# Kernel tuning notes

Hardware: AMD Instinct MI355X
Metric: run time of the kernel (lower is better)

Reference implementation:

```python
import jax, jax.numpy as jnp
import numpy as np

B, T, S, D = 8, 32, 256, 1024


def setup_inputs() -> dict:
    key = jax.random.key(0)
    ks = jax.random.split(key, 10)
    scale = 1.0 / np.sqrt(D)
    return {
        "source1": jax.random.normal(ks[0], (B, T, D), jnp.float32),
        "source2": jax.random.normal(ks[1], (B, T, D), jnp.float32),
        "memory_bank": jax.random.normal(ks[2], (B, S, D), jnp.float32),
        "source_masks1": jnp.ones((B, T), jnp.float32),
        "source_masks2": jnp.ones((B, T), jnp.float32),
        "W_q1": jax.random.normal(ks[3], (D, D), jnp.float32) * scale,
        "b_q1": jnp.zeros((D,), jnp.float32),
        "W_q2": jax.random.normal(ks[4], (D, D), jnp.float32) * scale,
        "b_q2": jnp.zeros((D,), jnp.float32),
        "W_cate": jax.random.normal(ks[5], (2, 2 * D), jnp.float32) * scale,
        "b_cate": jnp.zeros((2,), jnp.float32),
        "W_v": jax.random.normal(ks[6], (D, D), jnp.float32) * scale,
    }


def reference(source1, source2, memory_bank, source_masks1, source_masks2,
              W_q1, b_q1, W_q2, b_q2, W_cate, b_cate, W_v):
    Bq, Tq, Dd = source1.shape
    # accumulate(): running prefix-mean over the segment axis, then mask.
    denom = jnp.arange(1, Tq + 1, dtype=source1.dtype)[None, :, None]
    s1 = (jnp.cumsum(source1, axis=1) / denom) * source_masks1[:, :, None]
    s2 = (jnp.cumsum(source2, axis=1) / denom) * source_masks2[:, :, None]
    # score(): gated attention scoring.
    q1 = s1 @ W_q1.T + b_q1  # [B,T,D]
    q2 = s2 @ W_q2.T + b_q2  # [B,T,D]
    # tanh gate broadcast over all (tgt, src) pairs -> [B,T,S,D]
    g = jnp.tanh(q1[:, :, None, :] + q2[:, :, None, :] + memory_bank[:, None, :, :])
    # sum_j (g @ W_v.T)[..., j] == g @ sum_j W_v[j, :]
    w_colsum = jnp.sum(W_v, axis=0)              # [D]
    sum_gate = g @ w_colsum                       # [B,T,S]
    # linear_cate(concat([h_s, sum_gate*h_s])) split into two halves
    pa = memory_bank @ W_cate[:, :Dd].T           # [B,S,2]
    pb = memory_bank @ W_cate[:, Dd:].T           # [B,S,2]
    out = pa[:, None, :, :] + sum_gate[..., None] * pb[:, None, :, :] + b_cate
    return out  # [B,T,S,2]
```

## Files before the change

kernel.cpp:

```cpp
#include <hip/hip_runtime.h>
#include <hip/hip_bf16.h>

#define Bb 8
#define Tt 32
#define Ss 256
#define Dd 1024

typedef short short8 __attribute__((ext_vector_type(8)));
typedef float floatx4 __attribute__((ext_vector_type(4)));

__device__ __forceinline__ float tanh_fast(float x) {
    x = fminf(12.f, fmaxf(-12.f, x));
    float e = __expf(2.f * x);
    return 1.f - 2.f * __builtin_amdgcn_rcpf(e + 1.f);
}

__device__ __forceinline__ float dot4(float4 a, float4 b) {
    return a.x * b.x + a.y * b.y + a.z * b.z + a.w * b.w;
}

__global__ __launch_bounds__(256) void prefix_kernel(
        const float* __restrict__ src1, const float* __restrict__ src2,
        const float* __restrict__ m1, const float* __restrict__ m2,
        __hip_bfloat16* __restrict__ s1b, __hip_bfloat16* __restrict__ s2b) {
    int idx = blockIdx.x * 256 + threadIdx.x;
    int srcsel = idx >> 13;
    int bd = idx & 8191;
    int b = bd >> 10, d = bd & 1023;
    const float* sp = srcsel ? src2 : src1;
    const float* mp = srcsel ? m2 : m1;
    __hip_bfloat16* op = srcsel ? s2b : s1b;
    float a = 0.f;
    for (int t = 0; t < Tt; t++) {
        a += sp[(size_t)(b * Tt + t) * Dd + d];
        float inv = __builtin_amdgcn_rcpf((float)(t + 1));
        op[(size_t)(b * Tt + t) * Dd + d] = __float2bfloat16(a * inv * mp[b * Tt + t]);
    }
}

__global__ __launch_bounds__(256) void castw_kernel(
        const float* __restrict__ W1, const float* __restrict__ W2,
        __hip_bfloat16* __restrict__ W1b, __hip_bfloat16* __restrict__ W2b) {
    int i = blockIdx.x * 256 + threadIdx.x;
    W1b[i] = __float2bfloat16(W1[i]);
    W2b[i] = __float2bfloat16(W2[i]);
}

__global__ __launch_bounds__(256) void wsum_part_kernel(
        const float* __restrict__ Wv, float* __restrict__ part) {
    int db = blockIdx.x & 3;
    int jc = blockIdx.x >> 2;
    int d = db * 256 + threadIdx.x;
    float a = 0.f;
    int j0 = jc * 64;
    for (int j = 0; j < 64; j++)
        a += Wv[(size_t)(j0 + j) * Dd + d];
    part[jc * Dd + d] = a;
}

__global__ __launch_bounds__(256) void wsum_final_kernel(
        const float* __restrict__ part, float* __restrict__ wsum) {
    int d = blockIdx.x * 256 + threadIdx.x;
    float a = 0.f;
    #pragma unroll
    for (int jc = 0; jc < 16; jc++)
        a += part[jc * Dd + d];
    wsum[d] = a;
}

__global__ __launch_bounds__(256) void gemm_kernel(
        const __hip_bfloat16* __restrict__ s1b, const __hip_bfloat16* __restrict__ s2b,
        const __hip_bfloat16* __restrict__ W1b, const __hip_bfloat16* __restrict__ W2b,
        const float* __restrict__ bq1, const float* __restrict__ bq2,
        float* __restrict__ q) {
    const int wave = threadIdx.x >> 6;
    const int lane = threadIdx.x & 63;
    const int tile = blockIdx.x * 4 + wave;
    const int m0 = (tile & 15) * 16;
    const int n0 = (tile >> 4) * 16;
    const int lm = lane & 15;
    const int quad = lane >> 4;

    floatx4 acc1 = {0.f, 0.f, 0.f, 0.f};
    floatx4 acc2 = {0.f, 0.f, 0.f, 0.f};
    const __hip_bfloat16* arow1 = s1b + (size_t)(m0 + lm) * Dd;
    const __hip_bfloat16* arow2 = s2b + (size_t)(m0 + lm) * Dd;
    const __hip_bfloat16* brow1 = W1b + (size_t)(n0 + lm) * Dd;
    const __hip_bfloat16* brow2 = W2b + (size_t)(n0 + lm) * Dd;

    for (int k0 = 0; k0 < Dd; k0 += 32) {
        const int off = k0 + quad * 8;
        short8 a1 = *(const short8*)(arow1 + off);
        short8 b1 = *(const short8*)(brow1 + off);
        acc1 = __builtin_amdgcn_mfma_f32_16x16x32_bf16(a1, b1, acc1, 0, 0, 0);
        short8 a2 = *(const short8*)(arow2 + off);
        short8 b2 = *(const short8*)(brow2 + off);
        acc2 = __builtin_amdgcn_mfma_f32_16x16x32_bf16(a2, b2, acc2, 0, 0, 0);
    }

    const int n = n0 + lm;
    const float bias = bq1[n] + bq2[n];
    #pragma unroll
    for (int r = 0; r < 4; r++) {
        const int m = m0 + quad * 4 + r;
        q[(size_t)m * Dd + n] = acc1[r] + acc2[r] + bias;
    }
}

__global__ __launch_bounds__(256) void out_kernel(
        const float* __restrict__ q, const float* __restrict__ mem,
        const float* __restrict__ wsum, const float* __restrict__ Wc,
        const float* __restrict__ bc, float* __restrict__ out) {
    const int wave = threadIdx.x >> 6;
    const int lane = threadIdx.x & 63;
    const int gid = blockIdx.x * 4 + wave;
    const int b = gid >> 8;
    const int s = gid & 255;
    const float* mrow = mem + (size_t)gid * Dd;

    float4 mv[4], wv[4];
    float pa0 = 0.f, pa1 = 0.f, pb0 = 0.f, pb1 = 0.f;
    #pragma unroll
    for (int j = 0; j < 4; j++) {
        const int d0 = j * 256 + lane * 4;
        mv[j] = *(const float4*)(mrow + d0);
        wv[j] = *(const float4*)(wsum + d0);
        float4 wa0 = *(const float4*)(Wc + d0);
        float4 wa1 = *(const float4*)(Wc + 2048 + d0);
        float4 wb0 = *(const float4*)(Wc + 1024 + d0);
        float4 wb1 = *(const float4*)(Wc + 2048 + 1024 + d0);
        pa0 += dot4(mv[j], wa0);
        pa1 += dot4(mv[j], wa1);
        pb0 += dot4(mv[j], wb0);
        pb1 += dot4(mv[j], wb1);
    }
    #pragma unroll
    for (int o = 32; o > 0; o >>= 1) {
        pa0 += __shfl_xor(pa0, o);
        pa1 += __shfl_xor(pa1, o);
        pb0 += __shfl_xor(pb0, o);
        pb1 += __shfl_xor(pb1, o);
    }
    const float bc0 = bc[0], bc1 = bc[1];

    for (int t = 0; t < Tt; t++) {
        const float* qrow = q + (size_t)(b * Tt + t) * Dd;
        float p = 0.f;
        #pragma unroll
        for (int j = 0; j < 4; j++) {
            const int d0 = j * 256 + lane * 4;
            float4 qv = *(const float4*)(qrow + d0);
            p = fmaf(tanh_fast(qv.x + mv[j].x), wv[j].x, p);
            p = fmaf(tanh_fast(qv.y + mv[j].y), wv[j].y, p);
            p = fmaf(tanh_fast(qv.z + mv[j].z), wv[j].z, p);
            p = fmaf(tanh_fast(qv.w + mv[j].w), wv[j].w, p);
        }
        #pragma unroll
        for (int o = 32; o > 0; o >>= 1) p += __shfl_xor(p, o);
        if (lane == 0) {
            const size_t o2 = ((size_t)(b * Tt + t) * Ss + s) * 2;
            out[o2]     = pa0 + p * pb0 + bc0;
            out[o2 + 1] = pa1 + p * pb1 + bc1;
        }
    }
}

extern "C" void kernel_launch(void* const* d_in, const int* in_sizes, int n_in,
                              void* d_out, int out_size, void* d_ws, size_t ws_size,
                              hipStream_t stream) {
    const float* src1 = (const float*)d_in[0];
    const float* src2 = (const float*)d_in[1];
    const float* mem  = (const float*)d_in[2];
    const float* m1   = (const float*)d_in[3];
    const float* m2   = (const float*)d_in[4];
    const float* Wq1  = (const float*)d_in[5];
    const float* bq1  = (const float*)d_in[6];
    const float* Wq2  = (const float*)d_in[7];
    const float* bq2  = (const float*)d_in[8];
    const float* Wc   = (const float*)d_in[9];
    const float* bc   = (const float*)d_in[10];
    const float* Wv   = (const float*)d_in[11];
    float* out = (float*)d_out;

    char* ws = (char*)d_ws;
    __hip_bfloat16* s1b = (__hip_bfloat16*)(ws);
    __hip_bfloat16* s2b = (__hip_bfloat16*)(ws + (512u << 10));
    __hip_bfloat16* W1b = (__hip_bfloat16*)(ws + (1u << 20));
    __hip_bfloat16* W2b = (__hip_bfloat16*)(ws + (3u << 20));
    float* q    = (float*)(ws + (5u << 20));
    float* wsum = (float*)(ws + (6u << 20));
    float* part = (float*)(ws + (6u << 20) + 4096);

    prefix_kernel<<<64, 256, 0, stream>>>(src1, src2, m1, m2, s1b, s2b);
    castw_kernel<<<4096, 256, 0, stream>>>(Wq1, Wq2, W1b, W2b);
    wsum_part_kernel<<<64, 256, 0, stream>>>(Wv, part);
    wsum_final_kernel<<<4, 256, 0, stream>>>(part, wsum);
    gemm_kernel<<<256, 256, 0, stream>>>(s1b, s2b, W1b, W2b, bq1, bq2, q);
    out_kernel<<<512, 256, 0, stream>>>(q, mem, wsum, Wc, bc, out);
}
```

Measured before the change: 147.1 us.

## Merge prep kernels, widen GEMM tiles, and rewrite tanh gate as sigmoid

The prefix-mean, weight cast and partial column-sum launches are folded into one prep kernel, and the final column-sum reduction is folded into the GEMM launch, cutting six launches to three. The GEMM now uses one wave per block, each computing a 16x32 tile and accumulating both weight products into shared accumulators. The tanh is rewritten as 1 - 2*sigmoid with the 2*log2(e) scale pre-applied to q and memory, so each element costs one exp2 and one rcp; the constant part is folded into per-row constants. The out kernel splits the T dimension in half to double the block count and processes two t rows per iteration with vectorised float2 stores. The clamp is removed, so exp2 can overflow to inf for large inputs, which rcp then maps to zero.

```diff
diff --git a/kernel.cpp b/kernel.cpp
--- a/kernel.cpp
+++ b/kernel.cpp
@@ -5,134 +5,155 @@
 #define Tt 32
 #define Ss 256
 #define Dd 1024
+#define SCALE 2.885390081777927f
 
 typedef short short8 __attribute__((ext_vector_type(8)));
 typedef float floatx4 __attribute__((ext_vector_type(4)));
 
-__device__ __forceinline__ float tanh_fast(float x) {
-    x = fminf(12.f, fmaxf(-12.f, x));
-    float e = __expf(2.f * x);
-    return 1.f - 2.f * __builtin_amdgcn_rcpf(e + 1.f);
+__device__ __forceinline__ unsigned short bf16b(float x) {
+    __hip_bfloat16 h = __float2bfloat16(x);
+    return *(unsigned short*)&h;
 }
 
 __device__ __forceinline__ float dot4(float4 a, float4 b) {
     return a.x * b.x + a.y * b.y + a.z * b.z + a.w * b.w;
 }
 
-__global__ __launch_bounds__(256) void prefix_kernel(
+__device__ __forceinline__ float sigm_term(float q, float m, float w, float acc) {
+    float e = __builtin_amdgcn_exp2f(q + m);
+    return fmaf(w, __builtin_amdgcn_rcpf(e + 1.f), acc);
+}
+
+__global__ __launch_bounds__(256) void prep_kernel(
         const float* __restrict__ src1, const float* __restrict__ src2,
         const float* __restrict__ m1, const float* __restrict__ m2,
-        __hip_bfloat16* __restrict__ s1b, __hip_bfloat16* __restrict__ s2b) {
-    int idx = blockIdx.x * 256 + threadIdx.x;
-    int srcsel = idx >> 13;
-    int bd = idx & 8191;
-    int b = bd >> 10, d = bd & 1023;
-    const float* sp = srcsel ? src2 : src1;
-    const float* mp = srcsel ? m2 : m1;
-    __hip_bfloat16* op = srcsel ? s2b : s1b;
-    float a = 0.f;
-    for (int t = 0; t < Tt; t++) {
-        a += sp[(size_t)(b * Tt + t) * Dd + d];
-        float inv = __builtin_amdgcn_rcpf((float)(t + 1));
-        op[(size_t)(b * Tt + t) * Dd + d] = __float2bfloat16(a * inv * mp[b * Tt + t]);
-    }
-}
-
-__global__ __launch_bounds__(256) void castw_kernel(
         const float* __restrict__ W1, const float* __restrict__ W2,
-        __hip_bfloat16* __restrict__ W1b, __hip_bfloat16* __restrict__ W2b) {
-    int i = blockIdx.x * 256 + threadIdx.x;
-    W1b[i] = __float2bfloat16(W1[i]);
-    W2b[i] = __float2bfloat16(W2[i]);
-}
-
-__global__ __launch_bounds__(256) void wsum_part_kernel(
-        const float* __restrict__ Wv, float* __restrict__ part) {
-    int db = blockIdx.x & 3;
-    int jc = blockIdx.x >> 2;
-    int d = db * 256 + threadIdx.x;
-    float a = 0.f;
-    int j0 = jc * 64;
-    for (int j = 0; j < 64; j++)
-        a += Wv[(size_t)(j0 + j) * Dd + d];
-    part[jc * Dd + d] = a;
-}
-
-__global__ __launch_bounds__(256) void wsum_final_kernel(
-        const float* __restrict__ part, float* __restrict__ wsum) {
-    int d = blockIdx.x * 256 + threadIdx.x;
-    float a = 0.f;
-    #pragma unroll
-    for (int jc = 0; jc < 16; jc++)
-        a += part[jc * Dd + d];
-    wsum[d] = a;
-}
-
-__global__ __launch_bounds__(256) void gemm_kernel(
-        const __hip_bfloat16* __restrict__ s1b, const __hip_bfloat16* __restrict__ s2b,
-        const __hip_bfloat16* __restrict__ W1b, const __hip_bfloat16* __restrict__ W2b,
+        const float* __restrict__ Wv,
+        unsigned short* __restrict__ W1b, unsigned short* __restrict__ W2b,
+        unsigned short* __restrict__ s1b, unsigned short* __restrict__ s2b,
+        float* __restrict__ part) {
+    const int blk = blockIdx.x, tid = threadIdx.x;
+    if (blk < 1024) {
+        const int idx = blk * 256 + tid;
+        float4 a = ((const float4*)W1)[idx];
+        float4 b = ((const float4*)W2)[idx];
+        ushort4 oa = { bf16b(a.x), bf16b(a.y), bf16b(a.z), bf16b(a.w) };
+        ushort4 ob = { bf16b(b.x), bf16b(b.y), bf16b(b.z), bf16b(b.w) };
+        ((ushort4*)W1b)[idx] = oa;
+        ((ushort4*)W2b)[idx] = ob;
+    } else if (blk < 1088) {
+        const int bb = blk - 1024;
+        const int db = bb & 3, jc = bb >> 2;
+        const int d = db * 256 + tid;
+        float a = 0.f;
+        const int j0 = jc * 64;
+        for (int j = 0; j < 64; j++)
+            a += Wv[(size_t)(j0 + j) * Dd + d];
+        part[jc * Dd + d] = a;
+    } else {
+        const int idx = (blk - 1088) * 256 + tid;
+        const int srcsel = idx >> 13;
+        const int bd = idx & 8191;
+        const int b = bd >> 10, d = bd & 1023;
+        const float* sp = srcsel ? src2 : src1;
+        const float* mp = srcsel ? m2 : m1;
+        unsigned short* op = srcsel ? s2b : s1b;
+        float a = 0.f;
+        for (int t = 0; t < Tt; t++) {
+            a += sp[(size_t)(b * Tt + t) * Dd + d];
+            float inv = __builtin_amdgcn_rcpf((float)(t + 1));
+            op[(size_t)(b * Tt + t) * Dd + d] = bf16b(a * inv * mp[b * Tt + t]);
+        }
+    }
+}
+
+__global__ __launch_bounds__(64) void gemm_kernel(
+        const unsigned short* __restrict__ s1b, const unsigned short* __restrict__ s2b,
+        const unsigned short* __restrict__ W1b, const unsigned short* __restrict__ W2b,
         const float* __restrict__ bq1, const float* __restrict__ bq2,
-        float* __restrict__ q) {
-    const int wave = threadIdx.x >> 6;
-    const int lane = threadIdx.x & 63;
-    const int tile = blockIdx.x * 4 + wave;
-    const int m0 = (tile & 15) * 16;
-    const int n0 = (tile >> 4) * 16;
+        const float* __restrict__ part,
+        float* __restrict__ qp, float* __restrict__ wsum) {
+    const int blk = blockIdx.x;
+    const int lane = threadIdx.x;
+    if (blk >= 512) {
+        const int d = (blk - 512) * 64 + lane;
+        float a = 0.f;
+        #pragma unroll
+        for (int jc = 0; jc < 16; jc++)
+            a += part[jc * Dd + d];
+        wsum[d] = a;
+        return;
+    }
+    const int m0 = (blk & 15) * 16;
+    const int n0 = (blk >> 4) * 32;
     const int lm = lane & 15;
     const int quad = lane >> 4;
 
+    floatx4 acc0 = {0.f, 0.f, 0.f, 0.f};
     floatx4 acc1 = {0.f, 0.f, 0.f, 0.f};
-    floatx4 acc2 = {0.f, 0.f, 0.f, 0.f};
-    const __hip_bfloat16* arow1 = s1b + (size_t)(m0 + lm) * Dd;
-    const __hip_bfloat16* arow2 = s2b + (size_t)(m0 + lm) * Dd;
-    const __hip_bfloat16* brow1 = W1b + (size_t)(n0 + lm) * Dd;
-    const __hip_bfloat16* brow2 = W2b + (size_t)(n0 + lm) * Dd;
-
+    const unsigned short* a1p = s1b + (size_t)(m0 + lm) * Dd;
+    const unsigned short* a2p = s2b + (size_t)(m0 + lm) * Dd;
+    const unsigned short* b1a = W1b + (size_t)(n0 + lm) * Dd;
+    const unsigned short* b1b = W1b + (size_t)(n0 + 16 + lm) * Dd;
+    const unsigned short* b2a = W2b + (size_t)(n0 + lm) * Dd;
+    const unsigned short* b2b = W2b + (size_t)(n0 + 16 + lm) * Dd;
+
+    #pragma unroll 2
     for (int k0 = 0; k0 < Dd; k0 += 32) {
         const int off = k0 + quad * 8;
-        short8 a1 = *(const short8*)(arow1 + off);
-        short8 b1 = *(const short8*)(brow1 + off);
-        acc1 = __builtin_amdgcn_mfma_f32_16x16x32_bf16(a1, b1, acc1, 0, 0, 0);
-        short8 a2 = *(const short8*)(arow2 + off);
-        short8 b2 = *(const short8*)(brow2 + off);
-        acc2 = __builtin_amdgcn_mfma_f32_16x16x32_bf16(a2, b2, acc2, 0, 0, 0);
-    }
-
-    const int n = n0 + lm;
-    const float bias = bq1[n] + bq2[n];
+        short8 a1 = *(const short8*)(a1p + off);
+        short8 a2 = *(const short8*)(a2p + off);
+        short8 vb1a = *(const short8*)(b1a + off);
+        short8 vb2a = *(const short8*)(b2a + off);
+        short8 vb1b = *(const short8*)(b1b + off);
+        short8 vb2b = *(const short8*)(b2b + off);
+        acc0 = __builtin_amdgcn_mfma_f32_16x16x32_bf16(a1, vb1a, acc0, 0, 0, 0);
+        acc1 = __builtin_amdgcn_mfma_f32_16x16x32_bf16(a1, vb1b, acc1, 0, 0, 0);
+        acc0 = __builtin_amdgcn_mfma_f32_16x16x32_bf16(a2, vb2a, acc0, 0, 0, 0);
+        acc1 = __builtin_amdgcn_mfma_f32_16x16x32_bf16(a2, vb2b, acc1, 0, 0, 0);
+    }
+
+    const int na = n0 + lm, nb = n0 + 16 + lm;
+    const float biasa = bq1[na] + bq2[na];
+    const float biasb = bq1[nb] + bq2[nb];
     #pragma unroll
     for (int r = 0; r < 4; r++) {
         const int m = m0 + quad * 4 + r;
-        q[(size_t)m * Dd + n] = acc1[r] + acc2[r] + bias;
+        qp[(size_t)m * Dd + na] = SCALE * (acc0[r] + biasa);
+        qp[(size_t)m * Dd + nb] = SCALE * (acc1[r] + biasb);
     }
 }
 
 __global__ __launch_bounds__(256) void out_kernel(
-        const float* __restrict__ q, const float* __restrict__ mem,
+        const float* __restrict__ qp, const float* __restrict__ mem,
         const float* __restrict__ wsum, const float* __restrict__ Wc,
         const float* __restrict__ bc, float* __restrict__ out) {
     const int wave = threadIdx.x >> 6;
     const int lane = threadIdx.x & 63;
     const int gid = blockIdx.x * 4 + wave;
-    const int b = gid >> 8;
-    const int s = gid & 255;
-    const float* mrow = mem + (size_t)gid * Dd;
+    const int half = gid >> 11;
+    const int bs = gid & 2047;
+    const int b = bs >> 8, s = bs & 255;
+    const float* mrow = mem + (size_t)bs * Dd;
 
     float4 mv[4], wv[4];
-    float pa0 = 0.f, pa1 = 0.f, pb0 = 0.f, pb1 = 0.f;
+    float pa0 = 0.f, pa1 = 0.f, pb0 = 0.f, pb1 = 0.f, Wl = 0.f;
     #pragma unroll
     for (int j = 0; j < 4; j++) {
         const int d0 = j * 256 + lane * 4;
-        mv[j] = *(const float4*)(mrow + d0);
+        float4 m_ = *(const float4*)(mrow + d0);
         wv[j] = *(const float4*)(wsum + d0);
+        Wl += wv[j].x + wv[j].y + wv[j].z + wv[j].w;
         float4 wa0 = *(const float4*)(Wc + d0);
         float4 wa1 = *(const float4*)(Wc + 2048 + d0);
         float4 wb0 = *(const float4*)(Wc + 1024 + d0);
-        float4 wb1 = *(const float4*)(Wc + 2048 + 1024 + d0);
-        pa0 += dot4(mv[j], wa0);
-        pa1 += dot4(mv[j], wa1);
-        pb0 += dot4(mv[j], wb0);
-        pb1 += dot4(mv[j], wb1);
+        float4 wb1 = *(const float4*)(Wc + 3072 + d0);
+        pa0 += dot4(m_, wa0);
+        pa1 += dot4(m_, wa1);
+        pb0 += dot4(m_, wb0);
+        pb1 += dot4(m_, wb1);
+        mv[j].x = m_.x * SCALE; mv[j].y = m_.y * SCALE;
+        mv[j].z = m_.z * SCALE; mv[j].w = m_.w * SCALE;
     }
     #pragma unroll
     for (int o = 32; o > 0; o >>= 1) {
@@ -140,27 +161,42 @@
         pa1 += __shfl_xor(pa1, o);
         pb0 += __shfl_xor(pb0, o);
         pb1 += __shfl_xor(pb1, o);
-    }
-    const float bc0 = bc[0], bc1 = bc[1];
-
-    for (int t = 0; t < Tt; t++) {
-        const float* qrow = q + (size_t)(b * Tt + t) * Dd;
-        float p = 0.f;
+        Wl  += __shfl_xor(Wl, o);
+    }
+    const float C0 = pa0 + Wl * pb0 + bc[0];
+    const float C1 = pa1 + Wl * pb1 + bc[1];
+    const float D0 = 2.f * pb0, D1 = 2.f * pb1;
+
+    const int t0 = half * 16;
+    for (int tp = 0; tp < 16; tp += 2) {
+        const float* q0 = qp + (size_t)(b * Tt + t0 + tp) * Dd;
+        const float* q1 = q0 + Dd;
+        float p0 = 0.f, p1 = 0.f;
         #pragma unroll
         for (int j = 0; j < 4; j++) {
             const int d0 = j * 256 + lane * 4;
-            float4 qv = *(const float4*)(qrow + d0);
-            p = fmaf(tanh_fast(qv.x + mv[j].x), wv[j].x, p);
-            p = fmaf(tanh_fast(qv.y + mv[j].y), wv[j].y, p);
-            p = fmaf(tanh_fast(qv.z + mv[j].z), wv[j].z, p);
-            p = fmaf(tanh_fast(qv.w + mv[j].w), wv[j].w, p);
+            float4 x0 = *(const float4*)(q0 + d0);
+            float4 x1 = *(const float4*)(q1 + d0);
+            p0 = sigm_term(x0.x, mv[j].x, wv[j].x, p0);
+            p0 = sigm_term(x0.y, mv[j].y, wv[j].y, p0);
+            p0 = sigm_term(x0.z, mv[j].z, wv[j].z, p0);
+            p0 = sigm_term(x0.w, mv[j].w, wv[j].w, p0);
+            p1 = sigm_term(x1.x, mv[j].x, wv[j].x, p1);
+            p1 = sigm_term(x1.y, mv[j].y, wv[j].y, p1);
+            p1 = sigm_term(x1.z, mv[j].z, wv[j].z, p1);
+            p1 = sigm_term(x1.w, mv[j].w, wv[j].w, p1);
         }
         #pragma unroll
-        for (int o = 32; o > 0; o >>= 1) p += __shfl_xor(p, o);
+        for (int o = 32; o > 0; o >>= 1) {
+            p0 += __shfl_xor(p0, o);
+            p1 += __shfl_xor(p1, o);
+        }
         if (lane == 0) {
-            const size_t o2 = ((size_t)(b * Tt + t) * Ss + s) * 2;
-            out[o2]     = pa0 + p * pb0 + bc0;
-            out[o2 + 1] = pa1 + p * pb1 + bc1;
+            const int tA = t0 + tp;
+            float2 oA = { C0 - D0 * p0, C1 - D1 * p0 };
+            float2 oB = { C0 - D0 * p1, C1 - D1 * p1 };
+            *(float2*)(out + ((size_t)(b * Tt + tA) * Ss + s) * 2) = oA;
+            *(float2*)(out + ((size_t)(b * Tt + tA + 1) * Ss + s) * 2) = oB;
         }
     }
 }
@@ -183,18 +219,16 @@
     float* out = (float*)d_out;
 
     char* ws = (char*)d_ws;
-    __hip_bfloat16* s1b = (__hip_bfloat16*)(ws);
-    __hip_bfloat16* s2b = (__hip_bfloat16*)(ws + (512u << 10));
-    __hip_bfloat16* W1b = (__hip_bfloat16*)(ws + (1u << 20));
-    __hip_bfloat16* W2b = (__hip_bfloat16*)(ws + (3u << 20));
-    float* q    = (float*)(ws + (5u << 20));
+    unsigned short* s1b = (unsigned short*)(ws);
+    unsigned short* s2b = (unsigned short*)(ws + (512u << 10));
+    unsigned short* W1b = (unsigned short*)(ws + (1u << 20));
+    unsigned short* W2b = (unsigned short*)(ws + (3u << 20));
+    float* qp   = (float*)(ws + (5u << 20));
     float* wsum = (float*)(ws + (6u << 20));
     float* part = (float*)(ws + (6u << 20) + 4096);
 
-    prefix_kernel<<<64, 256, 0, stream>>>(src1, src2, m1, m2, s1b, s2b);
-    castw_kernel<<<4096, 256, 0, stream>>>(Wq1, Wq2, W1b, W2b);
-    wsum_part_kernel<<<64, 256, 0, stream>>>(Wv, part);
-    wsum_final_kernel<<<4, 256, 0, stream>>>(part, wsum);
-    gemm_kernel<<<256, 256, 0, stream>>>(s1b, s2b, W1b, W2b, bq1, bq2, q);
-    out_kernel<<<512, 256, 0, stream>>>(q, mem, wsum, Wc, bc, out);
-}
+    prep_kernel<<<1152, 256, 0, stream>>>(src1, src2, m1, m2, Wq1, Wq2, Wv,
+                                          W1b, W2b, s1b, s2b, part);
+    gemm_kernel<<<528, 64, 0, stream>>>(s1b, s2b, W1b, W2b, bq1, bq2, part, qp, wsum);
+    out_kernel<<<1024, 256, 0, stream>>>(qp, mem, wsum, Wc, bc, out);
+}
```

Measured after the change: 128.7 us. -12.5%, faster.
